# Optimization experiments

Hardware: AMD Instinct MI355X
Metric: run time of the kernel (lower is better)

The kernel has to match this reference:

```python
import jax, jax.numpy as jnp
import numpy as np

N_NODES = 100000
N_EDGES = 1600000
IN_DIM, HID_DIM, OUT_DIM = 128, 128, 64


def setup_inputs() -> dict:
    key = jax.random.key(0)
    k1, k2, k3, k4 = jax.random.split(key, 4)
    x = jax.random.normal(k1, (N_NODES, IN_DIM), dtype=jnp.float32)
    edge_index = jax.random.randint(k2, (2, N_EDGES), 0, N_NODES, dtype=jnp.int64)
    W1 = jax.random.normal(k3, (IN_DIM, HID_DIM), dtype=jnp.float32) * (1.0 / np.sqrt(IN_DIM))
    b1 = jnp.zeros((HID_DIM,), dtype=jnp.float32)
    W2 = jax.random.normal(k4, (HID_DIM, OUT_DIM), dtype=jnp.float32) * (1.0 / np.sqrt(HID_DIM))
    b2 = jnp.zeros((OUT_DIM,), dtype=jnp.float32)
    return {"x": x, "edge_index": edge_index, "W1": W1, "b1": b1, "W2": W2, "b2": b2}


def _gcn_conv(h, src, dst, norm, W, b, n_nodes):
    # Dense transform first (PyG GCNConv order), then gather-scatter aggregation.
    h = h @ W                                   # [N, out]
    msg = h[src] * norm[:, None]                # [E, out] gather + scale
    out = jax.ops.segment_sum(msg, dst, num_segments=n_nodes)  # scatter-add
    return out + b


def reference(x, edge_index, W1, b1, W2, b2):
    src, dst = edge_index[0], edge_index[1]
    n = x.shape[0]
    # symmetric normalization: deg from in-degree (unit edge weights), no self loops
    deg = jax.ops.segment_sum(jnp.ones_like(src, dtype=x.dtype), dst, num_segments=n)
    deg_inv_sqrt = jnp.where(deg > 0, jax.lax.rsqrt(jnp.maximum(deg, 1.0)), 0.0)
    norm = deg_inv_sqrt[src] * deg_inv_sqrt[dst]  # [E]
    h = jax.nn.relu(_gcn_conv(x, src, dst, norm, W1, b1, n))
    # dropout is identity in eval mode
    out = _gcn_conv(h, src, dst, norm, W2, b2, n)
    return out
```

## Files before the change

kernel.cpp:

```cpp
#include <hip/hip_runtime.h>
#include <stdint.h>

#define NN 100000
#define NE 1600000
#define K_DIM 128

#define BSH 7
#define NBKT ((NN + (1 << BSH) - 1) >> BSH)
#define EPT 32
#define BIN_CHUNK (256 * EPT)
#define BIN_BLOCKS ((NE + BIN_CHUNK - 1) / BIN_CHUNK)
#define GEMM_BLOCKS ((NN + 63) / 64)
#define CAP 4096
#define PADE 2301000

typedef unsigned int uint32;
typedef unsigned short ushort16;
typedef __attribute__((ext_vector_type(8))) short bf16x8;
typedef __attribute__((ext_vector_type(4))) float f32x4;

__device__ __forceinline__ ushort16 f2bf(float f) {
    uint32 u = __float_as_uint(f);
    u += 0x7fffu + ((u >> 16) & 1u);
    return (ushort16)(u >> 16);
}
__device__ __forceinline__ float bf_lo(uint32 u) { return __uint_as_float(u << 16); }
__device__ __forceinline__ float bf_hi(uint32 u) { return __uint_as_float(u & 0xffff0000u); }

#define ACC8(v) do { \
    a0 += bf_lo((v).x); a1 += bf_hi((v).x); \
    a2 += bf_lo((v).y); a3 += bf_hi((v).y); \
    a4 += bf_lo((v).z); a5 += bf_hi((v).z); \
    a6 += bf_lo((v).w); a7 += bf_hi((v).w); } while (0)

#define ACC8S(v,d) do { \
    a0 = fmaf(d, bf_lo((v).x), a0); a1 = fmaf(d, bf_hi((v).x), a1); \
    a2 = fmaf(d, bf_lo((v).y), a2); a3 = fmaf(d, bf_hi((v).y), a3); \
    a4 = fmaf(d, bf_lo((v).z), a4); a5 = fmaf(d, bf_hi((v).z), a5); \
    a6 = fmaf(d, bf_lo((v).w), a6); a7 = fmaf(d, bf_hi((v).w), a7); } while (0)

__device__ __forceinline__ bf16x8 ld_frag8(const ushort16* p) {
    uint2 lo = *(const uint2*)p;
    uint2 hi = *(const uint2*)(p + 4);
    union { uint32 u[4]; bf16x8 v; } x;
    x.u[0] = lo.x; x.u[1] = lo.y; x.u[2] = hi.x; x.u[3] = hi.y;
    return x.v;
}

__global__ __launch_bounds__(256) void binxgemm_kernel(
        const int* __restrict__ ei, int* __restrict__ gcursor,
        uint32* __restrict__ staging,
        const float* __restrict__ x, const float* __restrict__ W1,
        ushort16* __restrict__ g1,
        const float* __restrict__ W2, ushort16* __restrict__ W2t, int M) {
    __shared__ __align__(16) char smem[50688];
    int tid = threadIdx.x;

    if (blockIdx.x < BIN_BLOCKS) {
        int* hist = (int*)smem;
        int* base = hist + NBKT;
        int e0 = blockIdx.x * BIN_CHUNK;

        for (int i = tid; i < NBKT; i += 256) hist[i] = 0;
        __syncthreads();

        #pragma unroll
        for (int k = 0; k < EPT; k++) {
            int e = e0 + k * 256 + tid;
            if (e < NE) {
                int d = ei[NE + e];
                atomicAdd(&hist[d >> BSH], 1);
            }
        }
        __syncthreads();

        for (int i = tid; i < NBKT; i += 256) {
            int c = hist[i];
            base[i] = c ? atomicAdd(&gcursor[i], c) : 0;
            hist[i] = 0;
        }
        __syncthreads();

        #pragma unroll
        for (int k = 0; k < EPT; k++) {
            int e = e0 + k * 256 + tid;
            if (e < NE) {
                int s = ei[e];
                int d = ei[NE + e];
                int b = d >> BSH;
                int off = atomicAdd(&hist[b], 1);
                staging[(size_t)b * CAP + base[b] + off] =
                    ((uint32)s << 7) | (uint32)(d & 127);
            }
        }
    } else if (blockIdx.x < BIN_BLOCKS + GEMM_BLOCKS) {
        constexpr int N = 128, BM = 64, K = K_DIM, LDA = 132, NT = N / 16;
        ushort16* As = (ushort16*)smem;
        ushort16* Bt = As + BM * LDA;
        int bid = (int)blockIdx.x - BIN_BLOCKS;
        int row0 = bid * BM;

        if (bid == 0 && tid < 64)
            ((uint32*)&g1[(size_t)NN * N])[tid] = 0u;

        #pragma unroll
        for (int c = 0; c < 8; c++) {
            int idx = c * 1024 + tid * 4;
            int r = idx >> 7, col = idx & 127;
            int ra = row0 + r;
            float4 v = (ra < M) ? *(const float4*)&x[(size_t)ra * K + col]
                                : make_float4(0.f, 0.f, 0.f, 0.f);
            ushort4 bq;
            bq.x = f2bf(v.x); bq.y = f2bf(v.y); bq.z = f2bf(v.z); bq.w = f2bf(v.w);
            *(ushort4*)&As[r * LDA + col] = bq;
        }
        #pragma unroll
        for (int c = 0; c < (K * N) / 1024; c++) {
            int idx = c * 1024 + tid * 4;
            int k = idx >> 7, n = idx & (N - 1);
            float4 v = *(const float4*)&W1[idx];
            Bt[(n + 0) * LDA + k] = f2bf(v.x);
            Bt[(n + 1) * LDA + k] = f2bf(v.y);
            Bt[(n + 2) * LDA + k] = f2bf(v.z);
            Bt[(n + 3) * LDA + k] = f2bf(v.w);
        }
        __syncthreads();

        int lane = tid & 63;
        int wv = tid >> 6;
        int m0 = wv * 16;
        int ml = lane & 15;
        int quad = lane >> 4;

        f32x4 acc[NT];
        #pragma unroll
        for (int i = 0; i < NT; i++) acc[i] = (f32x4){0.f, 0.f, 0.f, 0.f};

        #pragma unroll
        for (int ks = 0; ks < 4; ks++) {
            int kof = ks * 32 + quad * 8;
            bf16x8 a = ld_frag8(&As[(m0 + ml) * LDA + kof]);
            #pragma unroll
            for (int nt = 0; nt < NT; nt++) {
                bf16x8 bb = ld_frag8(&Bt[(nt * 16 + ml) * LDA + kof]);
                acc[nt] = __builtin_amdgcn_mfma_f32_16x16x32_bf16(a, bb, acc[nt], 0, 0, 0);
            }
        }

        #pragma unroll
        for (int r = 0; r < 4; r++) {
            int row = row0 + m0 + quad * 4 + r;
            if (row < M) {
                #pragma unroll
                for (int nt = 0; nt < NT; nt++)
                    g1[(size_t)row * N + nt * 16 + ml] = f2bf(acc[nt][r]);
            }
        }
    } else {
        #pragma unroll
        for (int c = 0; c < 8; c++) {
            int idx = c * 1024 + tid * 4;
            int k = idx >> 6, n = idx & 63;
            float4 v = *(const float4*)&W2[idx];
            W2t[(n + 0) * 128 + k] = f2bf(v.x);
            W2t[(n + 1) * 128 + k] = f2bf(v.y);
            W2t[(n + 2) * 128 + k] = f2bf(v.z);
            W2t[(n + 3) * 128 + k] = f2bf(v.w);
        }
    }
}

__global__ __launch_bounds__(256) void bucket_finish_kernel(
        const uint32* __restrict__ staging, const int* __restrict__ gcursor,
        int* __restrict__ gedge, int* __restrict__ deg, float* __restrict__ dis,
        int* __restrict__ row_start, int* __restrict__ ssrc) {
    __shared__ uint32 pairs[CAP];
    __shared__ int cnt[1 << BSH];
    __shared__ int sb[1 << BSH];
    __shared__ int cur[1 << BSH];
    __shared__ int pend[1 << BSH];
    __shared__ int bbase;
    int b = blockIdx.x;
    int node0 = b << BSH;
    int tid = threadIdx.x;
    int n_edges = gcursor[b];

    if (tid < (1 << BSH)) cnt[tid] = 0;
    __syncthreads();

    for (int i = tid; i < n_edges; i += 256) {
        uint32 p = staging[(size_t)b * CAP + i];
        pairs[i] = p;
        atomicAdd(&cnt[p & 127u], 1);
    }
    __syncthreads();

    int p = 0;
    if (tid < (1 << BSH)) {
        int node = node0 + tid;
        int c = cnt[tid];
        if (node < NN) {
            deg[node] = c;
            dis[node] = (c > 0) ? rsqrtf((float)c) : 0.0f;
            p = (c + 7) & ~7;
        } else if (node == NN) {
            dis[NN] = 0.0f;
        }
        sb[tid] = p;
    }
    __syncthreads();
    #pragma unroll
    for (int off = 1; off < (1 << BSH); off <<= 1) {
        int t = (tid >= off && tid < (1 << BSH)) ? sb[tid - off] : 0;
        __syncthreads();
        if (tid < (1 << BSH)) sb[tid] += t;
        __syncthreads();
    }
    if (tid == (1 << BSH) - 1) bbase = atomicAdd(gedge, sb[tid]);
    __syncthreads();

    if (tid < (1 << BSH)) {
        int rs = bbase + sb[tid] - p;
        cur[tid] = rs;
        pend[tid] = rs + p;
        int node = node0 + tid;
        if (node < NN) row_start[node] = rs;
    }
    __syncthreads();

    for (int i = tid; i < n_edges; i += 256) {
        uint32 pr = pairs[i];
        int off = atomicAdd(&cur[pr & 127u], 1);
        ssrc[off] = (int)(pr >> 7);
    }
    __syncthreads();

    if (tid < (1 << BSH)) {
        int node = node0 + tid;
        if (node < NN) {
            for (int q = cur[tid]; q < pend[tid]; q++) ssrc[q] = NN;
        }
    }
}

__global__ __launch_bounds__(256) void agg128f_kernel(
        const ushort16* __restrict__ g1, const int* __restrict__ row_start,
        const int* __restrict__ deg, const int* __restrict__ ssrc,
        const float* __restrict__ dis, const float* __restrict__ b1,
        const ushort16* __restrict__ W2t, ushort16* __restrict__ g2) {
    constexpr int LDA = 132;
    __shared__ ushort16 H[32 * LDA];
    __shared__ float sdis[32];

    int tid = threadIdx.x;
    int lane = tid & 63, wv = tid >> 6;
    int node0 = blockIdx.x * 32;

    if (blockIdx.x == 0 && tid < 32)
        ((uint32*)&g2[(size_t)NN * 64])[tid] = 0u;

    int fl = lane & 15;
    int q  = lane >> 4;
    int laneoff = fl * 16;
    const char* gb = (const char*)g1;

    for (int it = 0; it < 8; it++) {
        int node = node0 + it * 4 + wv;
        int beg = row_start[node];
        int ecount = (deg[node] + 7) & ~7;
        float sc = dis[node];

        int ecl = (ecount < 64) ? ecount : 64;
        bool act = lane < ecl;
        int idx = act ? ssrc[beg + lane] : (int)NN;
        float dsv = act ? dis[idx] : 0.f;

        float a0 = 0.f, a1 = 0.f, a2 = 0.f, a3 = 0.f;
        float a4 = 0.f, a5 = 0.f, a6 = 0.f, a7 = 0.f;

        int nb = ecl >> 3;
        int b = 0;
        for (; b + 2 <= nb; b += 2) {
            int s0a = __shfl(idx, b * 8 + q);
            int s1a = __shfl(idx, b * 8 + 4 + q);
            int s0b = __shfl(idx, b * 8 + 8 + q);
            int s1b = __shfl(idx, b * 8 + 12 + q);
            float d0a = __shfl(dsv, b * 8 + q);
            float d1a = __shfl(dsv, b * 8 + 4 + q);
            float d0b = __shfl(dsv, b * 8 + 8 + q);
            float d1b = __shfl(dsv, b * 8 + 12 + q);
            uint4 v0a = *(const uint4*)(gb + (((uint32)s0a << 8) + laneoff));
            uint4 v1a = *(const uint4*)(gb + (((uint32)s1a << 8) + laneoff));
            uint4 v0b = *(const uint4*)(gb + (((uint32)s0b << 8) + laneoff));
            uint4 v1b = *(const uint4*)(gb + (((uint32)s1b << 8) + laneoff));
            ACC8S(v0a, d0a); ACC8S(v1a, d1a); ACC8S(v0b, d0b); ACC8S(v1b, d1b);
        }
        if (b < nb) {
            int s0 = __shfl(idx, b * 8 + q);
            int s1 = __shfl(idx, b * 8 + 4 + q);
            float d0 = __shfl(dsv, b * 8 + q);
            float d1 = __shfl(dsv, b * 8 + 4 + q);
            uint4 v0 = *(const uint4*)(gb + (((uint32)s0 << 8) + laneoff));
            uint4 v1 = *(const uint4*)(gb + (((uint32)s1 << 8) + laneoff));
            ACC8S(v0, d0); ACC8S(v1, d1);
        }
        for (int e = beg + 64; e < beg + ecount; e += 8) {
            int idx2 = ssrc[e + (lane & 7)];
            float dsv2 = dis[idx2];
            int s0 = __shfl(idx2, q);
            int s1 = __shfl(idx2, 4 + q);
            float d0 = __shfl(dsv2, q);
            float d1 = __shfl(dsv2, 4 + q);
            uint4 v0 = *(const uint4*)(gb + (((uint32)s0 << 8) + laneoff));
            uint4 v1 = *(const uint4*)(gb + (((uint32)s1 << 8) + laneoff));
            ACC8S(v0, d0); ACC8S(v1, d1);
        }

        a0 += __shfl_xor(a0, 16); a1 += __shfl_xor(a1, 16);
        a2 += __shfl_xor(a2, 16); a3 += __shfl_xor(a3, 16);
        a4 += __shfl_xor(a4, 16); a5 += __shfl_xor(a5, 16);
        a6 += __shfl_xor(a6, 16); a7 += __shfl_xor(a7, 16);
        a0 += __shfl_xor(a0, 32); a1 += __shfl_xor(a1, 32);
        a2 += __shfl_xor(a2, 32); a3 += __shfl_xor(a3, 32);
        a4 += __shfl_xor(a4, 32); a5 += __shfl_xor(a5, 32);
        a6 += __shfl_xor(a6, 32); a7 += __shfl_xor(a7, 32);

        int hrow = it * 4 + wv;
        if (lane == 0) sdis[hrow] = sc;
        if (lane < 16) {
            float4 bA = *(const float4*)&b1[fl * 8];
            float4 bB = *(const float4*)&b1[fl * 8 + 4];
            float o0 = fmaxf(sc * a0 + bA.x, 0.f);
            float o1 = fmaxf(sc * a1 + bA.y, 0.f);
            float o2 = fmaxf(sc * a2 + bA.z, 0.f);
            float o3 = fmaxf(sc * a3 + bA.w, 0.f);
            float o4 = fmaxf(sc * a4 + bB.x, 0.f);
            float o5 = fmaxf(sc * a5 + bB.y, 0.f);
            float o6 = fmaxf(sc * a6 + bB.z, 0.f);
            float o7 = fmaxf(sc * a7 + bB.w, 0.f);
            uint32 p0 = ((uint32)f2bf(o1) << 16) | (uint32)f2bf(o0);
            uint32 p1 = ((uint32)f2bf(o3) << 16) | (uint32)f2bf(o2);
            uint32 p2 = ((uint32)f2bf(o5) << 16) | (uint32)f2bf(o4);
            uint32 p3 = ((uint32)f2bf(o7) << 16) | (uint32)f2bf(o6);
            *(uint2*)&H[hrow * LDA + fl * 8]     = make_uint2(p0, p1);
            *(uint2*)&H[hrow * LDA + fl * 8 + 4] = make_uint2(p2, p3);
        }
    }
    __syncthreads();

    int m0 = (wv & 1) * 16;
    int nt0 = (wv >> 1) * 2;
    int ml = lane & 15;
    int quad = lane >> 4;

    f32x4 acc[2];
    acc[0] = (f32x4){0.f, 0.f, 0.f, 0.f};
    acc[1] = (f32x4){0.f, 0.f, 0.f, 0.f};

    #pragma unroll
    for (int ks = 0; ks < 4; ks++) {
        int kof = ks * 32 + quad * 8;
        bf16x8 a = ld_frag8(&H[(m0 + ml) * LDA + kof]);
        #pragma unroll
        for (int t = 0; t < 2; t++) {
            union { uint4 u; bf16x8 v; } bw;
            bw.u = *(const uint4*)&W2t[((nt0 + t) * 16 + ml) * 128 + kof];
            acc[t] = __builtin_amdgcn_mfma_f32_16x16x32_bf16(a, bw.v, acc[t], 0, 0, 0);
        }
    }

    #pragma unroll
    for (int r = 0; r < 4; r++) {
        int row = m0 + quad * 4 + r;
        float s = sdis[row];
        size_t gbase = (size_t)(node0 + row) * 64;
        #pragma unroll
        for (int t = 0; t < 2; t++)
            g2[gbase + (nt0 + t) * 16 + ml] = f2bf(acc[t][r] * s);
    }
}

__global__ __launch_bounds__(256) void agg64_kernel(
        const ushort16* __restrict__ g, const int* __restrict__ row_start,
        const int* __restrict__ deg, const int* __restrict__ ssrc,
        const float* __restrict__ dis, const float* __restrict__ bias,
        float* __restrict__ out) {
    int wave = (blockIdx.x * 256 + threadIdx.x) >> 6;
    int lane = threadIdx.x & 63;
    int half = lane >> 5;
    int l2 = lane & 31;
    int node = wave * 2 + half;
    if (node >= NN) return;

    int beg = row_start[node];
    int ecount = (deg[node] + 7) & ~7;
    float sc = dis[node];

    int fl = l2 & 7;
    int q  = l2 >> 3;
    int laneoff = fl * 16;

    int idx = ssrc[beg + l2];

    float a0 = 0.f, a1 = 0.f, a2 = 0.f, a3 = 0.f;
    float a4 = 0.f, a5 = 0.f, a6 = 0.f, a7 = 0.f;

    const char* gb = (const char*)g;
    int nb = ((ecount < 32) ? ecount : 32) >> 3;
    int b = 0;
    for (; b + 2 <= nb; b += 2) {
        int s0a = __shfl(idx, half * 32 + b * 8 + q);
        int s1a = __shfl(idx, half * 32 + b * 8 + 4 + q);
        int s0b = __shfl(idx, half * 32 + b * 8 + 8 + q);
        int s1b = __shfl(idx, half * 32 + b * 8 + 12 + q);
        uint4 v0a = *(const uint4*)(gb + (((uint32)s0a << 7) + laneoff));
        uint4 v1a = *(const uint4*)(gb + (((uint32)s1a << 7) + laneoff));
        uint4 v0b = *(const uint4*)(gb + (((uint32)s0b << 7) + laneoff));
        uint4 v1b = *(const uint4*)(gb + (((uint32)s1b << 7) + laneoff));
        ACC8(v0a); ACC8(v1a); ACC8(v0b); ACC8(v1b);
    }
    if (b < nb) {
        int s0 = __shfl(idx, half * 32 + b * 8 + q);
        int s1 = __shfl(idx, half * 32 + b * 8 + 4 + q);
        uint4 v0 = *(const uint4*)(gb + (((uint32)s0 << 7) + laneoff));
        uint4 v1 = *(const uint4*)(gb + (((uint32)s1 << 7) + laneoff));
        ACC8(v0); ACC8(v1);
    }
    for (int e = beg + 32; e < beg + ecount; e += 8) {
        int idx2 = ssrc[e + (l2 & 7)];
        int s0 = __shfl(idx2, half * 32 + q);
        int s1 = __shfl(idx2, half * 32 + 4 + q);
        uint4 v0 = *(const uint4*)(gb + (((uint32)s0 << 7) + laneoff));
        uint4 v1 = *(const uint4*)(gb + (((uint32)s1 << 7) + laneoff));
        ACC8(v0); ACC8(v1);
    }

    a0 += __shfl_xor(a0, 8);  a1 += __shfl_xor(a1, 8);
    a2 += __shfl_xor(a2, 8);  a3 += __shfl_xor(a3, 8);
    a4 += __shfl_xor(a4, 8);  a5 += __shfl_xor(a5, 8);
    a6 += __shfl_xor(a6, 8);  a7 += __shfl_xor(a7, 8);
    a0 += __shfl_xor(a0, 16); a1 += __shfl_xor(a1, 16);
    a2 += __shfl_xor(a2, 16); a3 += __shfl_xor(a3, 16);
    a4 += __shfl_xor(a4, 16); a5 += __shfl_xor(a5, 16);
    a6 += __shfl_xor(a6, 16); a7 += __shfl_xor(a7, 16);

    if (l2 < 8) {
        float4 bA = *(const float4*)&bias[fl * 8];
        float4 bB = *(const float4*)&bias[fl * 8 + 4];
        float4 oA = make_float4(sc * a0 + bA.x, sc * a1 + bA.y,
                                sc * a2 + bA.z, sc * a3 + bA.w);
        float4 oB = make_float4(sc * a4 + bB.x, sc * a5 + bB.y,
                                sc * a6 + bB.z, sc * a7 + bB.w);
        *(float4*)&out[(size_t)node * 64 + fl * 8]     = oA;
        *(float4*)&out[(size_t)node * 64 + fl * 8 + 4] = oB;
    }
}

extern "C" void kernel_launch(void* const* d_in, const int* in_sizes, int n_in,
                              void* d_out, int out_size, void* d_ws, size_t ws_size,
                              hipStream_t stream) {
    const float* x  = (const float*)d_in[0];
    const int*   ei = (const int*)d_in[1];
    const float* W1 = (const float*)d_in[2];
    const float* b1 = (const float*)d_in[3];
    const float* W2 = (const float*)d_in[4];
    const float* b2 = (const float*)d_in[5];
    float* out = (float*)d_out;

    char* ws = (char*)d_ws;
    size_t off = 0;
    auto alloc = [&](size_t bytes) {
        void* p = ws + off;
        off = (off + bytes + 255) & ~(size_t)255;
        return p;
    };

    int*      deg_i      = (int*)alloc(NN * 4);
    float*    dis        = (float*)alloc((NN + 1) * 4);
    int*      row_start  = (int*)alloc(NN * 4);
    int*      gcursor    = (int*)alloc((NBKT + 1) * 4);
    ushort16* W2t        = (ushort16*)alloc(64 * 128 * 2);
    int*      ssrc       = (int*)alloc((size_t)PADE * 4);
    ushort16* g1         = (ushort16*)alloc((size_t)(NN + 1) * 128 * 2);
    char*     big        = (char*)alloc((size_t)NBKT * CAP * 4);
    uint32*   staging    = (uint32*)big;
    ushort16* g2         = (ushort16*)big;
    int*      gedge      = gcursor + NBKT;

    hipMemsetAsync(gcursor, 0, (NBKT + 1) * 4, stream);

    binxgemm_kernel<<<BIN_BLOCKS + GEMM_BLOCKS + 1, 256, 0, stream>>>(
        ei, gcursor, staging, x, W1, g1, W2, W2t, NN);

    bucket_finish_kernel<<<NBKT, 256, 0, stream>>>(
        staging, gcursor, gedge, deg_i, dis, row_start, ssrc);

    agg128f_kernel<<<NN / 32, 256, 0, stream>>>(
        g1, row_start, deg_i, ssrc, dis, b1, W2t, g2);

    const int AGG2_BLOCKS = (NN / 2 + 3) / 4;
    agg64_kernel<<<AGG2_BLOCKS, 256, 0, stream>>>(g2, row_start, deg_i, ssrc, dis, b2, out);
}
```

Before: 270.6 us.

## Shrink fused aggregation block to four nodes with one MFMA tile per wave

The fused layer-1 aggregation plus W2 GEMM kernel now gives each block 4 nodes (one per wave) instead of 32 nodes processed in 8 sequential iterations. The grid grows eightfold and each wave computes one 16-column MFMA tile over a 4-row H buffer (rows replicated across the 16 M lanes). The intent is more parallelism and latency hiding for the irregular gather, and no serial per-block loop. In exchange, W2t fragments are reloaded per block, three quarters of each MFMA's rows are redundant, and only a quarter of the lanes write results.

```diff
diff --git a/kernel.cpp b/kernel.cpp
--- a/kernel.cpp
+++ b/kernel.cpp
@@ -27,17 +27,17 @@
 __device__ __forceinline__ float bf_lo(uint32 u) { return __uint_as_float(u << 16); }
 __device__ __forceinline__ float bf_hi(uint32 u) { return __uint_as_float(u & 0xffff0000u); }
 
+#define ACC8S(v,d) do { \
+    a0 = fmaf(d, bf_lo((v).x), a0); a1 = fmaf(d, bf_hi((v).x), a1); \
+    a2 = fmaf(d, bf_lo((v).y), a2); a3 = fmaf(d, bf_hi((v).y), a3); \
+    a4 = fmaf(d, bf_lo((v).z), a4); a5 = fmaf(d, bf_hi((v).z), a5); \
+    a6 = fmaf(d, bf_lo((v).w), a6); a7 = fmaf(d, bf_hi((v).w), a7); } while (0)
+
 #define ACC8(v) do { \
     a0 += bf_lo((v).x); a1 += bf_hi((v).x); \
     a2 += bf_lo((v).y); a3 += bf_hi((v).y); \
     a4 += bf_lo((v).z); a5 += bf_hi((v).z); \
     a6 += bf_lo((v).w); a7 += bf_hi((v).w); } while (0)
-
-#define ACC8S(v,d) do { \
-    a0 = fmaf(d, bf_lo((v).x), a0); a1 = fmaf(d, bf_hi((v).x), a1); \
-    a2 = fmaf(d, bf_lo((v).y), a2); a3 = fmaf(d, bf_hi((v).y), a3); \
-    a4 = fmaf(d, bf_lo((v).z), a4); a5 = fmaf(d, bf_hi((v).z), a5); \
-    a6 = fmaf(d, bf_lo((v).w), a6); a7 = fmaf(d, bf_hi((v).w), a7); } while (0)
 
 __device__ __forceinline__ bf16x8 ld_frag8(const ushort16* p) {
     uint2 lo = *(const uint2*)p;
@@ -249,134 +249,120 @@
         const float* __restrict__ dis, const float* __restrict__ b1,
         const ushort16* __restrict__ W2t, ushort16* __restrict__ g2) {
     constexpr int LDA = 132;
-    __shared__ ushort16 H[32 * LDA];
-    __shared__ float sdis[32];
+    __shared__ ushort16 H[4 * LDA];
+    __shared__ float sdis[4];
 
     int tid = threadIdx.x;
     int lane = tid & 63, wv = tid >> 6;
-    int node0 = blockIdx.x * 32;
+    int node = blockIdx.x * 4 + wv;
 
     if (blockIdx.x == 0 && tid < 32)
         ((uint32*)&g2[(size_t)NN * 64])[tid] = 0u;
+
+    int beg = row_start[node];
+    int ecount = (deg[node] + 7) & ~7;
+    float sc = dis[node];
 
     int fl = lane & 15;
     int q  = lane >> 4;
     int laneoff = fl * 16;
     const char* gb = (const char*)g1;
 
-    for (int it = 0; it < 8; it++) {
-        int node = node0 + it * 4 + wv;
-        int beg = row_start[node];
-        int ecount = (deg[node] + 7) & ~7;
-        float sc = dis[node];
-
-        int ecl = (ecount < 64) ? ecount : 64;
-        bool act = lane < ecl;
-        int idx = act ? ssrc[beg + lane] : (int)NN;
-        float dsv = act ? dis[idx] : 0.f;
-
-        float a0 = 0.f, a1 = 0.f, a2 = 0.f, a3 = 0.f;
-        float a4 = 0.f, a5 = 0.f, a6 = 0.f, a7 = 0.f;
-
-        int nb = ecl >> 3;
-        int b = 0;
-        for (; b + 2 <= nb; b += 2) {
-            int s0a = __shfl(idx, b * 8 + q);
-            int s1a = __shfl(idx, b * 8 + 4 + q);
-            int s0b = __shfl(idx, b * 8 + 8 + q);
-            int s1b = __shfl(idx, b * 8 + 12 + q);
-            float d0a = __shfl(dsv, b * 8 + q);
-            float d1a = __shfl(dsv, b * 8 + 4 + q);
-            float d0b = __shfl(dsv, b * 8 + 8 + q);
-            float d1b = __shfl(dsv, b * 8 + 12 + q);
-            uint4 v0a = *(const uint4*)(gb + (((uint32)s0a << 8) + laneoff));
-            uint4 v1a = *(const uint4*)(gb + (((uint32)s1a << 8) + laneoff));
-            uint4 v0b = *(const uint4*)(gb + (((uint32)s0b << 8) + laneoff));
-            uint4 v1b = *(const uint4*)(gb + (((uint32)s1b << 8) + laneoff));
-            ACC8S(v0a, d0a); ACC8S(v1a, d1a); ACC8S(v0b, d0b); ACC8S(v1b, d1b);
-        }
-        if (b < nb) {
-            int s0 = __shfl(idx, b * 8 + q);
-            int s1 = __shfl(idx, b * 8 + 4 + q);
-            float d0 = __shfl(dsv, b * 8 + q);
-            float d1 = __shfl(dsv, b * 8 + 4 + q);
-            uint4 v0 = *(const uint4*)(gb + (((uint32)s0 << 8) + laneoff));
-            uint4 v1 = *(const uint4*)(gb + (((uint32)s1 << 8) + laneoff));
-            ACC8S(v0, d0); ACC8S(v1, d1);
-        }
-        for (int e = beg + 64; e < beg + ecount; e += 8) {
-            int idx2 = ssrc[e + (lane & 7)];
-            float dsv2 = dis[idx2];
-            int s0 = __shfl(idx2, q);
-            int s1 = __shfl(idx2, 4 + q);
-            float d0 = __shfl(dsv2, q);
-            float d1 = __shfl(dsv2, 4 + q);
-            uint4 v0 = *(const uint4*)(gb + (((uint32)s0 << 8) + laneoff));
-            uint4 v1 = *(const uint4*)(gb + (((uint32)s1 << 8) + laneoff));
-            ACC8S(v0, d0); ACC8S(v1, d1);
-        }
-
-        a0 += __shfl_xor(a0, 16); a1 += __shfl_xor(a1, 16);
-        a2 += __shfl_xor(a2, 16); a3 += __shfl_xor(a3, 16);
-        a4 += __shfl_xor(a4, 16); a5 += __shfl_xor(a5, 16);
-        a6 += __shfl_xor(a6, 16); a7 += __shfl_xor(a7, 16);
-        a0 += __shfl_xor(a0, 32); a1 += __shfl_xor(a1, 32);
-        a2 += __shfl_xor(a2, 32); a3 += __shfl_xor(a3, 32);
-        a4 += __shfl_xor(a4, 32); a5 += __shfl_xor(a5, 32);
-        a6 += __shfl_xor(a6, 32); a7 += __shfl_xor(a7, 32);
-
-        int hrow = it * 4 + wv;
-        if (lane == 0) sdis[hrow] = sc;
-        if (lane < 16) {
-            float4 bA = *(const float4*)&b1[fl * 8];
-            float4 bB = *(const float4*)&b1[fl * 8 + 4];
-            float o0 = fmaxf(sc * a0 + bA.x, 0.f);
-            float o1 = fmaxf(sc * a1 + bA.y, 0.f);
-            float o2 = fmaxf(sc * a2 + bA.z, 0.f);
-            float o3 = fmaxf(sc * a3 + bA.w, 0.f);
-            float o4 = fmaxf(sc * a4 + bB.x, 0.f);
-            float o5 = fmaxf(sc * a5 + bB.y, 0.f);
-            float o6 = fmaxf(sc * a6 + bB.z, 0.f);
-            float o7 = fmaxf(sc * a7 + bB.w, 0.f);
-            uint32 p0 = ((uint32)f2bf(o1) << 16) | (uint32)f2bf(o0);
-            uint32 p1 = ((uint32)f2bf(o3) << 16) | (uint32)f2bf(o2);
-            uint32 p2 = ((uint32)f2bf(o5) << 16) | (uint32)f2bf(o4);
-            uint32 p3 = ((uint32)f2bf(o7) << 16) | (uint32)f2bf(o6);
-            *(uint2*)&H[hrow * LDA + fl * 8]     = make_uint2(p0, p1);
-            *(uint2*)&H[hrow * LDA + fl * 8 + 4] = make_uint2(p2, p3);
-        }
-    }
-    __syncthreads();
-
-    int m0 = (wv & 1) * 16;
-    int nt0 = (wv >> 1) * 2;
+    int ecl = (ecount < 64) ? ecount : 64;
+    bool act = lane < ecl;
+    int idx = act ? ssrc[beg + lane] : (int)NN;
+    float dsv = act ? dis[idx] : 0.f;
+
+    float a0 = 0.f, a1 = 0.f, a2 = 0.f, a3 = 0.f;
+    float a4 = 0.f, a5 = 0.f, a6 = 0.f, a7 = 0.f;
+
+    int nb = ecl >> 3;
+    int b = 0;
+    for (; b + 2 <= nb; b += 2) {
+        int s0a = __shfl(idx, b * 8 + q);
+        int s1a = __shfl(idx, b * 8 + 4 + q);
+        int s0b = __shfl(idx, b * 8 + 8 + q);
+        int s1b = __shfl(idx, b * 8 + 12 + q);
+        float d0a = __shfl(dsv, b * 8 + q);
+        float d1a = __shfl(dsv, b * 8 + 4 + q);
+        float d0b = __shfl(dsv, b * 8 + 8 + q);
+        float d1b = __shfl(dsv, b * 8 + 12 + q);
+        uint4 v0a = *(const uint4*)(gb + (((uint32)s0a << 8) + laneoff));
+        uint4 v1a = *(const uint4*)(gb + (((uint32)s1a << 8) + laneoff));
+        uint4 v0b = *(const uint4*)(gb + (((uint32)s0b << 8) + laneoff));
+        uint4 v1b = *(const uint4*)(gb + (((uint32)s1b << 8) + laneoff));
+        ACC8S(v0a, d0a); ACC8S(v1a, d1a); ACC8S(v0b, d0b); ACC8S(v1b, d1b);
+    }
+    if (b < nb) {
+        int s0 = __shfl(idx, b * 8 + q);
+        int s1 = __shfl(idx, b * 8 + 4 + q);
+        float d0 = __shfl(dsv, b * 8 + q);
+        float d1 = __shfl(dsv, b * 8 + 4 + q);
+        uint4 v0 = *(const uint4*)(gb + (((uint32)s0 << 8) + laneoff));
+        uint4 v1 = *(const uint4*)(gb + (((uint32)s1 << 8) + laneoff));
+        ACC8S(v0, d0); ACC8S(v1, d1);
+    }
+    for (int e = beg + 64; e < beg + ecount; e += 8) {
+        int idx2 = ssrc[e + (lane & 7)];
+        float dsv2 = dis[idx2];
+        int s0 = __shfl(idx2, q);
+        int s1 = __shfl(idx2, 4 + q);
+        float d0 = __shfl(dsv2, q);
+        float d1 = __shfl(dsv2, 4 + q);
+        uint4 v0 = *(const uint4*)(gb + (((uint32)s0 << 8) + laneoff));
+        uint4 v1 = *(const uint4*)(gb + (((uint32)s1 << 8) + laneoff));
+        ACC8S(v0, d0); ACC8S(v1, d1);
+    }
+
+    a0 += __shfl_xor(a0, 16); a1 += __shfl_xor(a1, 16);
+    a2 += __shfl_xor(a2, 16); a3 += __shfl_xor(a3, 16);
+    a4 += __shfl_xor(a4, 16); a5 += __shfl_xor(a5, 16);
+    a6 += __shfl_xor(a6, 16); a7 += __shfl_xor(a7, 16);
+    a0 += __shfl_xor(a0, 32); a1 += __shfl_xor(a1, 32);
+    a2 += __shfl_xor(a2, 32); a3 += __shfl_xor(a3, 32);
+    a4 += __shfl_xor(a4, 32); a5 += __shfl_xor(a5, 32);
+    a6 += __shfl_xor(a6, 32); a7 += __shfl_xor(a7, 32);
+
+    if (lane == 0) sdis[wv] = sc;
+    if (lane < 16) {
+        float4 bA = *(const float4*)&b1[fl * 8];
+        float4 bB = *(const float4*)&b1[fl * 8 + 4];
+        float o0 = fmaxf(sc * a0 + bA.x, 0.f);
+        float o1 = fmaxf(sc * a1 + bA.y, 0.f);
+        float o2 = fmaxf(sc * a2 + bA.z, 0.f);
+        float o3 = fmaxf(sc * a3 + bA.w, 0.f);
+        float o4 = fmaxf(sc * a4 + bB.x, 0.f);
+        float o5 = fmaxf(sc * a5 + bB.y, 0.f);
+        float o6 = fmaxf(sc * a6 + bB.z, 0.f);
+        float o7 = fmaxf(sc * a7 + bB.w, 0.f);
+        uint32 p0 = ((uint32)f2bf(o1) << 16) | (uint32)f2bf(o0);
+        uint32 p1 = ((uint32)f2bf(o3) << 16) | (uint32)f2bf(o2);
+        uint32 p2 = ((uint32)f2bf(o5) << 16) | (uint32)f2bf(o4);
+        uint32 p3 = ((uint32)f2bf(o7) << 16) | (uint32)f2bf(o6);
+        *(uint2*)&H[wv * LDA + fl * 8]     = make_uint2(p0, p1);
+        *(uint2*)&H[wv * LDA + fl * 8 + 4] = make_uint2(p2, p3);
+    }
+    __syncthreads();
+
     int ml = lane & 15;
     int quad = lane >> 4;
 
-    f32x4 acc[2];
-    acc[0] = (f32x4){0.f, 0.f, 0.f, 0.f};
-    acc[1] = (f32x4){0.f, 0.f, 0.f, 0.f};
-
+    f32x4 acc = (f32x4){0.f, 0.f, 0.f, 0.f};
     #pragma unroll
     for (int ks = 0; ks < 4; ks++) {
         int kof = ks * 32 + quad * 8;
-        bf16x8 a = ld_frag8(&H[(m0 + ml) * LDA + kof]);
-        #pragma unroll
-        for (int t = 0; t < 2; t++) {
-            union { uint4 u; bf16x8 v; } bw;
-            bw.u = *(const uint4*)&W2t[((nt0 + t) * 16 + ml) * 128 + kof];
-            acc[t] = __builtin_amdgcn_mfma_f32_16x16x32_bf16(a, bw.v, acc[t], 0, 0, 0);
-        }
-    }
-
-    #pragma unroll
-    for (int r = 0; r < 4; r++) {
-        int row = m0 + quad * 4 + r;
-        float s = sdis[row];
-        size_t gbase = (size_t)(node0 + row) * 64;
-        #pragma unroll
-        for (int t = 0; t < 2; t++)
-            g2[gbase + (nt0 + t) * 16 + ml] = f2bf(acc[t][r] * s);
+        bf16x8 a = ld_frag8(&H[(ml & 3) * LDA + kof]);
+        union { uint4 u; bf16x8 v; } bw;
+        bw.u = *(const uint4*)&W2t[(wv * 16 + ml) * 128 + kof];
+        acc = __builtin_amdgcn_mfma_f32_16x16x32_bf16(a, bw.v, acc, 0, 0, 0);
+    }
+
+    if (quad == 0) {
+        #pragma unroll
+        for (int r = 0; r < 4; r++) {
+            float s = sdis[r];
+            g2[(size_t)(blockIdx.x * 4 + r) * 64 + wv * 16 + ml] = f2bf(acc[r] * s);
+        }
     }
 }
 
@@ -495,7 +481,7 @@
     bucket_finish_kernel<<<NBKT, 256, 0, stream>>>(
         staging, gcursor, gedge, deg_i, dis, row_start, ssrc);
 
-    agg128f_kernel<<<NN / 32, 256, 0, stream>>>(
+    agg128f_kernel<<<NN / 4, 256, 0, stream>>>(
         g1, row_start, deg_i, ssrc, dis, b1, W2t, g2);
 
     const int AGG2_BLOCKS = (NN / 2 + 3) / 4;
```

Result: slower. 288.6 us (+6.7%).
